# Performance work log

Measured on AMD Instinct MI355X. Metric: run time of the kernel, lower is better.

Reference implementation:

```python
import jax, jax.numpy as jnp
import numpy as np

NOTE_UNITS = 3
NUM_NOTES = 48
NUM_FEATURES = 256
NUM_UNITS = 256
BATCH = 4096


def _uniform(key, shape, k):
    return jax.random.uniform(key, shape, jnp.float32, -k, k)


def setup_inputs() -> dict:
    key = jax.random.key(0)
    ks = jax.random.split(key, 12)
    k = 1.0 / np.sqrt(NUM_UNITS)
    in0 = NUM_FEATURES + NOTE_UNITS  # layer-0 input: features concat shifted notes
    return {
        "note_features": jax.random.normal(ks[0], (BATCH, NUM_NOTES, NUM_FEATURES), jnp.float32),
        "condition_notes": jax.random.uniform(ks[1], (BATCH, NUM_NOTES, NOTE_UNITS), jnp.float32),
        "W_ih0": _uniform(ks[2], (4 * NUM_UNITS, in0), k),
        "W_hh0": _uniform(ks[3], (4 * NUM_UNITS, NUM_UNITS), k),
        "b_ih0": _uniform(ks[4], (4 * NUM_UNITS,), k),
        "b_hh0": _uniform(ks[5], (4 * NUM_UNITS,), k),
        "W_ih1": _uniform(ks[6], (4 * NUM_UNITS, NUM_UNITS), k),
        "W_hh1": _uniform(ks[7], (4 * NUM_UNITS, NUM_UNITS), k),
        "b_ih1": _uniform(ks[8], (4 * NUM_UNITS,), k),
        "b_hh1": _uniform(ks[9], (4 * NUM_UNITS,), k),
        "W_out": _uniform(ks[10], (NOTE_UNITS, NUM_UNITS), k),
        "b_out": _uniform(ks[11], (NOTE_UNITS,), k),
    }


def _lstm_cell(x, h, c, W_ih, W_hh, b_ih, b_hh):
    # torch.nn.LSTMCell gate order: i, f, g, o (each NUM_UNITS rows)
    gates = x @ W_ih.T + h @ W_hh.T + (b_ih + b_hh)
    i, f, g, o = jnp.split(gates, 4, axis=-1)
    c_new = jax.nn.sigmoid(f) * c + jax.nn.sigmoid(i) * jnp.tanh(g)
    h_new = jax.nn.sigmoid(o) * jnp.tanh(c_new)
    return h_new, c_new


def reference(note_features, condition_notes, W_ih0, W_hh0, b_ih0, b_hh0,
              W_ih1, W_hh1, b_ih1, b_hh1, W_out, b_out):
    temperature = 1.0
    B = note_features.shape[0]
    # shift condition notes right by one (teacher forcing)
    zero_pad = jnp.zeros((B, 1, NOTE_UNITS), note_features.dtype)
    shifted = jnp.concatenate([zero_pad, condition_notes], axis=1)[:, :-1]
    x_all = jnp.concatenate([note_features, shifted], axis=2)  # [B, N, F+3]
    xs = jnp.transpose(x_all, (1, 0, 2))  # [N, B, F+3] for scan over notes

    h0 = jnp.zeros((B, NUM_UNITS), note_features.dtype)
    init = (h0, h0, h0, h0)  # (h_l0, c_l0, h_l1, c_l1)

    def step(carry, x_n):
        h0_, c0_, h1_, c1_ = carry
        h0n, c0n = _lstm_cell(x_n, h0_, c0_, W_ih0, W_hh0, b_ih0, b_hh0)
        h1n, c1n = _lstm_cell(h0n, h1_, c1_, W_ih1, W_hh1, b_ih1, b_hh1)
        return (h0n, c0n, h1n, c1n), h1n

    _, hs = jax.lax.scan(step, init, xs)  # [N, B, U]
    hs = jnp.transpose(hs, (1, 0, 2))  # [B, N, U]
    out = hs @ W_out.T + b_out  # [B, N, 3]
    prob = jax.nn.sigmoid(out[:, :, 0:2] / temperature)
    return jnp.concatenate([prob, out[:, :, 2:3]], axis=2)
```

## Files before the change

kernel.cpp:

```cpp
#include <hip/hip_runtime.h>

typedef _Float16 half8 __attribute__((ext_vector_type(8)));
typedef _Float16 half4 __attribute__((ext_vector_type(4)));
typedef float f32x4 __attribute__((ext_vector_type(4)));

#define NSTEP 48
#define MT 16
#define LDX 264
#define LDH0 296
#define LDH1 264

__device__ __forceinline__ float sigm(float x) { return 1.0f / (1.0f + __expf(-x)); }
__device__ __forceinline__ float tanh_f(float x) {
  float ax = fabsf(x);
  float e = __expf(-2.0f * ax);
  float t = (1.0f - e) / (1.0f + e);
  return copysignf(t, x);
}

__global__ void prep_weights(const float* __restrict__ Wih0, const float* __restrict__ Whh0,
                             const float* __restrict__ bih0, const float* __restrict__ bhh0,
                             const float* __restrict__ Wih1, const float* __restrict__ Whh1,
                             const float* __restrict__ bih1, const float* __restrict__ bhh1,
                             _Float16* __restrict__ W0p, _Float16* __restrict__ W1p,
                             float* __restrict__ b0, float* __restrict__ b1) {
  int n = blockIdx.x;
  int c = n >> 8, u = n & 255, w = u >> 4, r = u & 15;
  for (int k = threadIdx.x; k < 544; k += 256) {
    int kt = k >> 5, kk = k & 31, q = kk >> 3, j = kk & 7;
    float val;
    if (k < 256) val = Wih0[n * 259 + k];
    else if (k < 512) val = Whh0[n * 256 + (k - 256)];
    else if (k < 515) val = Wih0[n * 259 + 256 + (k - 512)];
    else val = 0.0f;
    W0p[((((w * 17 + kt) * 4 + c) * 64) + q * 16 + r) * 8 + j] = (_Float16)val;
  }
  for (int k = threadIdx.x; k < 512; k += 256) {
    int kt = k >> 5, kk = k & 31, q = kk >> 3, j = kk & 7;
    float val = (k < 256) ? Wih1[n * 256 + k] : Whh1[n * 256 + (k - 256)];
    W1p[((((w * 16 + kt) * 4 + c) * 64) + q * 16 + r) * 8 + j] = (_Float16)val;
  }
  if (threadIdx.x == 0) { b0[n] = bih0[n] + bhh0[n]; b1[n] = bih1[n] + bhh1[n]; }
}

__global__ __launch_bounds__(1024, 4)
void noteaxis_main(const float* __restrict__ nf, const float* __restrict__ cond,
                   const _Float16* __restrict__ W0p, const _Float16* __restrict__ W1p,
                   const float* __restrict__ b0g, const float* __restrict__ b1g,
                   const float* __restrict__ Wout, const float* __restrict__ bout,
                   float* __restrict__ out) {
  __shared__ __align__(16) _Float16 lds_x[MT][LDX];
  __shared__ __align__(16) _Float16 lds_h0[MT][LDH0];
  __shared__ __align__(16) _Float16 lds_h1[MT][LDH1];
  __shared__ float lds_part[16][MT][3];

  const int tid = threadIdx.x;
  const int w = tid >> 6;
  const int lane = tid & 63;
  const int r = lane & 15;
  const int q = lane >> 4;
  const int u = w * 16 + r;
  const int row0 = blockIdx.x * MT;

  for (int i = tid; i < MT * LDH0; i += 1024) ((_Float16*)lds_h0)[i] = (_Float16)0.0f;
  for (int i = tid; i < MT * LDH1; i += 1024) ((_Float16*)lds_h1)[i] = (_Float16)0.0f;

  float b0c[4], b1c[4];
#pragma unroll
  for (int c = 0; c < 4; ++c) { b0c[c] = b0g[c * 256 + u]; b1c[c] = b1g[c * 256 + u]; }
  const float wov0 = Wout[u], wov1 = Wout[256 + u], wov2 = Wout[512 + u];
  const float bo0 = bout[0], bo1 = bout[1], bo2 = bout[2];

  float c0s[4], c1s[4];
#pragma unroll
  for (int g = 0; g < 4; ++g) { c0s[g] = 0.0f; c1s[g] = 0.0f; }

  const _Float16* pW0 = W0p + (size_t)w * (17 * 4 * 512) + lane * 8;
  const _Float16* pW1 = W1p + (size_t)w * (16 * 4 * 512) + lane * 8;

  f32x4 acc[4];
  half8 Ba[4], Bc[4];

  auto loadW = [&](half8* d, const _Float16* base, int ktc4) {
#pragma unroll
    for (int c = 0; c < 4; ++c) d[c] = *(const half8*)(base + (ktc4 + c) * 512);
  };
  auto mfma4 = [&](half8 a, const half8* B) {
#pragma unroll
    for (int c = 0; c < 4; ++c)
      acc[c] = __builtin_amdgcn_mfma_f32_16x16x32_f16(a, B[c], acc[c], 0, 0, 0);
  };

  __syncthreads();

#pragma unroll 1
  for (int n = 0; n < NSTEP; ++n) {
    {
      const float4 xv = *(const float4*)(nf + ((size_t)(row0 + w) * NSTEP + n) * 256 + lane * 4);
      half4 hx = { (_Float16)xv.x, (_Float16)xv.y, (_Float16)xv.z, (_Float16)xv.w };
      *(half4*)&lds_x[w][lane * 4] = hx;
    }
    if (tid < MT) {
      float s0 = 0.f, s1 = 0.f, s2 = 0.f;
      if (n > 0) {
        const float* cp = cond + ((size_t)(row0 + tid) * NSTEP + (n - 1)) * 3;
        s0 = cp[0]; s1 = cp[1]; s2 = cp[2];
      }
      lds_h0[tid][256] = (_Float16)s0;
      lds_h0[tid][257] = (_Float16)s1;
      lds_h0[tid][258] = (_Float16)s2;
    }
    __syncthreads();

#pragma unroll
    for (int c = 0; c < 4; ++c) { f32x4 bz = {b0c[c], b0c[c], b0c[c], b0c[c]}; acc[c] = bz; }

#pragma unroll 2
    for (int kt = 0; kt < 8; kt += 2) {
      loadW(Ba, pW0, kt * 4);
      loadW(Bc, pW0, kt * 4 + 4);
      mfma4(*(const half8*)&lds_x[r][kt * 32 + q * 8], Ba);
      mfma4(*(const half8*)&lds_x[r][kt * 32 + 32 + q * 8], Bc);
    }
#pragma unroll 2
    for (int kt = 0; kt < 8; kt += 2) {
      loadW(Ba, pW0, 32 + kt * 4);
      loadW(Bc, pW0, 32 + kt * 4 + 4);
      mfma4(*(const half8*)&lds_h0[r][kt * 32 + q * 8], Ba);
      mfma4(*(const half8*)&lds_h0[r][kt * 32 + 32 + q * 8], Bc);
    }
    loadW(Ba, pW0, 64);
    mfma4(*(const half8*)&lds_h0[r][256 + q * 8], Ba);

    __syncthreads();

#pragma unroll
    for (int g = 0; g < 4; ++g) {
      float i_ = acc[0][g], f_ = acc[1][g], g_ = acc[2][g], o_ = acc[3][g];
      float cc = sigm(f_) * c0s[g] + sigm(i_) * tanh_f(g_);
      c0s[g] = cc;
      lds_h0[q * 4 + g][u] = (_Float16)(sigm(o_) * tanh_f(cc));
    }
    __syncthreads();

#pragma unroll
    for (int c = 0; c < 4; ++c) { f32x4 bz = {b1c[c], b1c[c], b1c[c], b1c[c]}; acc[c] = bz; }

#pragma unroll 2
    for (int kt = 0; kt < 8; kt += 2) {
      loadW(Ba, pW1, kt * 4);
      loadW(Bc, pW1, kt * 4 + 4);
      mfma4(*(const half8*)&lds_h0[r][kt * 32 + q * 8], Ba);
      mfma4(*(const half8*)&lds_h0[r][kt * 32 + 32 + q * 8], Bc);
    }
#pragma unroll 2
    for (int kt = 0; kt < 8; kt += 2) {
      loadW(Ba, pW1, 32 + kt * 4);
      loadW(Bc, pW1, 32 + kt * 4 + 4);
      mfma4(*(const half8*)&lds_h1[r][kt * 32 + q * 8], Ba);
      mfma4(*(const half8*)&lds_h1[r][kt * 32 + 32 + q * 8], Bc);
    }

    __syncthreads();

    float part[4][3];
#pragma unroll
    for (int g = 0; g < 4; ++g) {
      float i_ = acc[0][g], f_ = acc[1][g], g_ = acc[2][g], o_ = acc[3][g];
      float cc = sigm(f_) * c1s[g] + sigm(i_) * tanh_f(g_);
      c1s[g] = cc;
      float hh = sigm(o_) * tanh_f(cc);
      lds_h1[q * 4 + g][u] = (_Float16)hh;
      part[g][0] = hh * wov0;
      part[g][1] = hh * wov1;
      part[g][2] = hh * wov2;
    }
#pragma unroll
    for (int g = 0; g < 4; ++g)
#pragma unroll
      for (int ch = 0; ch < 3; ++ch) {
        float p = part[g][ch];
        p += __shfl_xor(p, 1);
        p += __shfl_xor(p, 2);
        p += __shfl_xor(p, 4);
        p += __shfl_xor(p, 8);
        part[g][ch] = p;
      }
    if (r == 0) {
#pragma unroll
      for (int g = 0; g < 4; ++g) {
        int m = q * 4 + g;
        lds_part[w][m][0] = part[g][0];
        lds_part[w][m][1] = part[g][1];
        lds_part[w][m][2] = part[g][2];
      }
    }
    __syncthreads();

    if (tid < MT * 3) {
      int m = tid / 3, ch = tid - m * 3;
      float s = (ch == 0 ? bo0 : (ch == 1 ? bo1 : bo2));
#pragma unroll
      for (int ww = 0; ww < 16; ++ww) s += lds_part[ww][m][ch];
      if (ch < 2) s = 1.0f / (1.0f + __expf(-s));
      out[((size_t)(row0 + m) * NSTEP + n) * 3 + ch] = s;
    }
  }
}

extern "C" void kernel_launch(void* const* d_in, const int* in_sizes, int n_in,
                              void* d_out, int out_size, void* d_ws, size_t ws_size,
                              hipStream_t stream) {
  const float* nf   = (const float*)d_in[0];
  const float* cond = (const float*)d_in[1];
  const float* Wih0 = (const float*)d_in[2];
  const float* Whh0 = (const float*)d_in[3];
  const float* bih0 = (const float*)d_in[4];
  const float* bhh0 = (const float*)d_in[5];
  const float* Wih1 = (const float*)d_in[6];
  const float* Whh1 = (const float*)d_in[7];
  const float* bih1 = (const float*)d_in[8];
  const float* bhh1 = (const float*)d_in[9];
  const float* Wout = (const float*)d_in[10];
  const float* bout = (const float*)d_in[11];
  float* out = (float*)d_out;

  _Float16* W0p = (_Float16*)d_ws;
  _Float16* W1p = W0p + 16 * 17 * 4 * 512;
  float* b0 = (float*)(W1p + 16 * 16 * 4 * 512);
  float* b1 = b0 + 1024;

  prep_weights<<<1024, 256, 0, stream>>>(Wih0, Whh0, bih0, bhh0, Wih1, Whh1, bih1, bhh1, W0p, W1p, b0, b1);
  noteaxis_main<<<256, 1024, 0, stream>>>(nf, cond, W0p, W1p, b0, b1, Wout, bout, out);
}
```

Baseline: 1.363 ms.

## Software-pipeline weight loads with triple buffering and cut per-step barriers

Replaces the paired weight-fragment loads with a three-deep rotating register buffer that prefetches weight tiles three k-steps ahead, including across the layer-0/layer-1 boundary and into the next time step. It prefetches the next note's features from global memory during the current step and moves the x/condition LDS writes and the output reduction into an existing barrier window, cutting per-step barriers from five to three. It also raises wave priority around the MFMA loops and uses a custom barrier macro. The goal is to hide global weight-load latency and barrier stalls, at the cost of more live registers, which could hurt occupancy under the 1024x4 launch bounds.

```diff
diff --git a/kernel.cpp b/kernel.cpp
--- a/kernel.cpp
+++ b/kernel.cpp
@@ -9,6 +9,10 @@
 #define LDX 264
 #define LDH0 296
 #define LDH1 264
+
+#define BAR() do { asm volatile("s_waitcnt lgkmcnt(0)" ::: "memory"); \
+                   __builtin_amdgcn_s_barrier();                      \
+                   __builtin_amdgcn_sched_barrier(0); } while (0)
 
 __device__ __forceinline__ float sigm(float x) { return 1.0f / (1.0f + __expf(-x)); }
 __device__ __forceinline__ float tanh_f(float x) {
@@ -79,60 +83,55 @@
   const _Float16* pW1 = W1p + (size_t)w * (16 * 4 * 512) + lane * 8;
 
   f32x4 acc[4];
-  half8 Ba[4], Bc[4];
-
-  auto loadW = [&](half8* d, const _Float16* base, int ktc4) {
-#pragma unroll
-    for (int c = 0; c < 4; ++c) d[c] = *(const half8*)(base + (ktc4 + c) * 512);
+  half8 Qb[3][4];
+
+  auto loadQ = [&](int buf, const _Float16* base, int t) {
+#pragma unroll
+    for (int c = 0; c < 4; ++c) Qb[buf][c] = *(const half8*)(base + (t * 4 + c) * 512);
   };
-  auto mfma4 = [&](half8 a, const half8* B) {
+  auto mfma4 = [&](half8 a, int buf) {
 #pragma unroll
     for (int c = 0; c < 4; ++c)
-      acc[c] = __builtin_amdgcn_mfma_f32_16x16x32_f16(a, B[c], acc[c], 0, 0, 0);
+      acc[c] = __builtin_amdgcn_mfma_f32_16x16x32_f16(a, Qb[buf][c], acc[c], 0, 0, 0);
   };
 
+  {
+    const float4 xv = *(const float4*)(nf + ((size_t)(row0 + w) * NSTEP + 0) * 256 + lane * 4);
+    half4 hx = { (_Float16)xv.x, (_Float16)xv.y, (_Float16)xv.z, (_Float16)xv.w };
+    *(half4*)&lds_x[w][lane * 4] = hx;
+  }
   __syncthreads();
+
+  loadQ(0, pW0, 0); loadQ(1, pW0, 1); loadQ(2, pW0, 2);
 
 #pragma unroll 1
   for (int n = 0; n < NSTEP; ++n) {
-    {
-      const float4 xv = *(const float4*)(nf + ((size_t)(row0 + w) * NSTEP + n) * 256 + lane * 4);
-      half4 hx = { (_Float16)xv.x, (_Float16)xv.y, (_Float16)xv.z, (_Float16)xv.w };
-      *(half4*)&lds_x[w][lane * 4] = hx;
-    }
+    const int np = (n + 1 < NSTEP) ? n + 1 : n;
+    const float4 xv = *(const float4*)(nf + ((size_t)(row0 + w) * NSTEP + np) * 256 + lane * 4);
+    float s0 = 0.f, s1 = 0.f, s2 = 0.f;
     if (tid < MT) {
-      float s0 = 0.f, s1 = 0.f, s2 = 0.f;
-      if (n > 0) {
-        const float* cp = cond + ((size_t)(row0 + tid) * NSTEP + (n - 1)) * 3;
-        s0 = cp[0]; s1 = cp[1]; s2 = cp[2];
-      }
-      lds_h0[tid][256] = (_Float16)s0;
-      lds_h0[tid][257] = (_Float16)s1;
-      lds_h0[tid][258] = (_Float16)s2;
-    }
-    __syncthreads();
+      const float* cp = cond + ((size_t)(row0 + tid) * NSTEP + n) * 3;
+      s0 = cp[0]; s1 = cp[1]; s2 = cp[2];
+    }
 
 #pragma unroll
     for (int c = 0; c < 4; ++c) { f32x4 bz = {b0c[c], b0c[c], b0c[c], b0c[c]}; acc[c] = bz; }
 
-#pragma unroll 2
-    for (int kt = 0; kt < 8; kt += 2) {
-      loadW(Ba, pW0, kt * 4);
-      loadW(Bc, pW0, kt * 4 + 4);
-      mfma4(*(const half8*)&lds_x[r][kt * 32 + q * 8], Ba);
-      mfma4(*(const half8*)&lds_x[r][kt * 32 + 32 + q * 8], Bc);
-    }
-#pragma unroll 2
-    for (int kt = 0; kt < 8; kt += 2) {
-      loadW(Ba, pW0, 32 + kt * 4);
-      loadW(Bc, pW0, 32 + kt * 4 + 4);
-      mfma4(*(const half8*)&lds_h0[r][kt * 32 + q * 8], Ba);
-      mfma4(*(const half8*)&lds_h0[r][kt * 32 + 32 + q * 8], Bc);
-    }
-    loadW(Ba, pW0, 64);
-    mfma4(*(const half8*)&lds_h0[r][256 + q * 8], Ba);
-
-    __syncthreads();
+    __builtin_amdgcn_s_setprio(1);
+#pragma unroll
+    for (int t = 0; t < 17; ++t) {
+      half8 a;
+      if (t < 8)       a = *(const half8*)&lds_x[r][t * 32 + q * 8];
+      else if (t < 16) a = *(const half8*)&lds_h0[r][(t - 8) * 32 + q * 8];
+      else             a = *(const half8*)&lds_h0[r][256 + q * 8];
+      mfma4(a, t % 3);
+      const int nt = t + 3;
+      if (nt < 17) loadQ(t % 3, pW0, nt);
+      else         loadQ(t % 3, pW1, nt - 17);
+    }
+    __builtin_amdgcn_s_setprio(0);
+
+    BAR();
 
 #pragma unroll
     for (int g = 0; g < 4; ++g) {
@@ -141,27 +140,42 @@
       c0s[g] = cc;
       lds_h0[q * 4 + g][u] = (_Float16)(sigm(o_) * tanh_f(cc));
     }
-    __syncthreads();
+    {
+      half4 hx = { (_Float16)xv.x, (_Float16)xv.y, (_Float16)xv.z, (_Float16)xv.w };
+      *(half4*)&lds_x[w][lane * 4] = hx;
+    }
+    if (tid < MT) {
+      lds_h0[tid][256] = (_Float16)s0;
+      lds_h0[tid][257] = (_Float16)s1;
+      lds_h0[tid][258] = (_Float16)s2;
+    }
+    if (n > 0 && tid < MT * 3) {
+      int m = tid / 3, ch = tid - m * 3;
+      float s = (ch == 0 ? bo0 : (ch == 1 ? bo1 : bo2));
+#pragma unroll
+      for (int ww = 0; ww < 16; ++ww) s += lds_part[ww][m][ch];
+      if (ch < 2) s = 1.0f / (1.0f + __expf(-s));
+      out[((size_t)(row0 + m) * NSTEP + (n - 1)) * 3 + ch] = s;
+    }
+
+    BAR();
 
 #pragma unroll
     for (int c = 0; c < 4; ++c) { f32x4 bz = {b1c[c], b1c[c], b1c[c], b1c[c]}; acc[c] = bz; }
 
-#pragma unroll 2
-    for (int kt = 0; kt < 8; kt += 2) {
-      loadW(Ba, pW1, kt * 4);
-      loadW(Bc, pW1, kt * 4 + 4);
-      mfma4(*(const half8*)&lds_h0[r][kt * 32 + q * 8], Ba);
-      mfma4(*(const half8*)&lds_h0[r][kt * 32 + 32 + q * 8], Bc);
-    }
-#pragma unroll 2
-    for (int kt = 0; kt < 8; kt += 2) {
-      loadW(Ba, pW1, 32 + kt * 4);
-      loadW(Bc, pW1, 32 + kt * 4 + 4);
-      mfma4(*(const half8*)&lds_h1[r][kt * 32 + q * 8], Ba);
-      mfma4(*(const half8*)&lds_h1[r][kt * 32 + 32 + q * 8], Bc);
-    }
-
-    __syncthreads();
+    __builtin_amdgcn_s_setprio(1);
+#pragma unroll
+    for (int t = 0; t < 16; ++t) {
+      half8 a = (t < 8) ? *(const half8*)&lds_h0[r][t * 32 + q * 8]
+                        : *(const half8*)&lds_h1[r][(t - 8) * 32 + q * 8];
+      mfma4(a, (t + 2) % 3);
+      const int nt = t + 3;
+      if (nt < 16) loadQ((t + 2) % 3, pW1, nt);
+      else         loadQ((t + 2) % 3, pW0, nt - 16);
+    }
+    __builtin_amdgcn_s_setprio(0);
+
+    BAR();
 
     float part[4][3];
 #pragma unroll
@@ -195,16 +209,16 @@
         lds_part[w][m][2] = part[g][2];
       }
     }
-    __syncthreads();
-
-    if (tid < MT * 3) {
-      int m = tid / 3, ch = tid - m * 3;
-      float s = (ch == 0 ? bo0 : (ch == 1 ? bo1 : bo2));
-#pragma unroll
-      for (int ww = 0; ww < 16; ++ww) s += lds_part[ww][m][ch];
-      if (ch < 2) s = 1.0f / (1.0f + __expf(-s));
-      out[((size_t)(row0 + m) * NSTEP + n) * 3 + ch] = s;
-    }
+  }
+
+  BAR();
+  if (tid < MT * 3) {
+    int m = tid / 3, ch = tid - m * 3;
+    float s = (ch == 0 ? bo0 : (ch == 1 ? bo1 : bo2));
+#pragma unroll
+    for (int ww = 0; ww < 16; ++ww) s += lds_part[ww][m][ch];
+    if (ch < 2) s = 1.0f / (1.0f + __expf(-s));
+    out[((size_t)(row0 + m) * NSTEP + (NSTEP - 1)) * 3 + ch] = s;
   }
 }
 
```

Measured after the change: 5.158 ms. 3.78x slower.

## Process 32 batch rows per block to reuse each weight fragment twice

Applied to the files above, without the earlier changes.

Doubles the rows per workgroup from 16 to 32 so every weight fragment loaded from global memory feeds two MFMA row tiles, with separate accumulators and cell states for each half. The grid is halved to 128 blocks, and the gate biases are staged in LDS instead of registers. This targets the per-step weight-streaming cost, but uses only half the CUs and raises register pressure.

```diff
diff --git a/kernel.cpp b/kernel.cpp
--- a/kernel.cpp
+++ b/kernel.cpp
@@ -5,7 +5,7 @@
 typedef float f32x4 __attribute__((ext_vector_type(4)));
 
 #define NSTEP 48
-#define MT 16
+#define MT 32
 #define LDX 264
 #define LDH0 296
 #define LDH1 264
@@ -53,6 +53,7 @@
   __shared__ __align__(16) _Float16 lds_h0[MT][LDH0];
   __shared__ __align__(16) _Float16 lds_h1[MT][LDH1];
   __shared__ float lds_part[16][MT][3];
+  __shared__ float lds_b0[1024], lds_b1[1024];
 
   const int tid = threadIdx.x;
   const int w = tid >> 6;
@@ -64,31 +65,32 @@
 
   for (int i = tid; i < MT * LDH0; i += 1024) ((_Float16*)lds_h0)[i] = (_Float16)0.0f;
   for (int i = tid; i < MT * LDH1; i += 1024) ((_Float16*)lds_h1)[i] = (_Float16)0.0f;
-
-  float b0c[4], b1c[4];
-#pragma unroll
-  for (int c = 0; c < 4; ++c) { b0c[c] = b0g[c * 256 + u]; b1c[c] = b1g[c * 256 + u]; }
+  lds_b0[tid] = b0g[tid];
+  lds_b1[tid] = b1g[tid];
+
   const float wov0 = Wout[u], wov1 = Wout[256 + u], wov2 = Wout[512 + u];
   const float bo0 = bout[0], bo1 = bout[1], bo2 = bout[2];
 
-  float c0s[4], c1s[4];
-#pragma unroll
-  for (int g = 0; g < 4; ++g) { c0s[g] = 0.0f; c1s[g] = 0.0f; }
+  float c0sA[4], c0sB[4], c1sA[4], c1sB[4];
+#pragma unroll
+  for (int g = 0; g < 4; ++g) { c0sA[g] = 0.0f; c0sB[g] = 0.0f; c1sA[g] = 0.0f; c1sB[g] = 0.0f; }
 
   const _Float16* pW0 = W0p + (size_t)w * (17 * 4 * 512) + lane * 8;
   const _Float16* pW1 = W1p + (size_t)w * (16 * 4 * 512) + lane * 8;
 
-  f32x4 acc[4];
+  f32x4 accA[4], accB[4];
   half8 Ba[4], Bc[4];
 
   auto loadW = [&](half8* d, const _Float16* base, int ktc4) {
 #pragma unroll
     for (int c = 0; c < 4; ++c) d[c] = *(const half8*)(base + (ktc4 + c) * 512);
   };
-  auto mfma4 = [&](half8 a, const half8* B) {
-#pragma unroll
-    for (int c = 0; c < 4; ++c)
-      acc[c] = __builtin_amdgcn_mfma_f32_16x16x32_f16(a, B[c], acc[c], 0, 0, 0);
+  auto mfmaD = [&](half8 aA, half8 aB, const half8* B) {
+#pragma unroll
+    for (int c = 0; c < 4; ++c) {
+      accA[c] = __builtin_amdgcn_mfma_f32_16x16x32_f16(aA, B[c], accA[c], 0, 0, 0);
+      accB[c] = __builtin_amdgcn_mfma_f32_16x16x32_f16(aB, B[c], accB[c], 0, 0, 0);
+    }
   };
 
   __syncthreads();
@@ -96,9 +98,12 @@
 #pragma unroll 1
   for (int n = 0; n < NSTEP; ++n) {
     {
-      const float4 xv = *(const float4*)(nf + ((size_t)(row0 + w) * NSTEP + n) * 256 + lane * 4);
-      half4 hx = { (_Float16)xv.x, (_Float16)xv.y, (_Float16)xv.z, (_Float16)xv.w };
-      *(half4*)&lds_x[w][lane * 4] = hx;
+      const float4 xa = *(const float4*)(nf + ((size_t)(row0 + w) * NSTEP + n) * 256 + lane * 4);
+      const float4 xb = *(const float4*)(nf + ((size_t)(row0 + 16 + w) * NSTEP + n) * 256 + lane * 4);
+      half4 ha = { (_Float16)xa.x, (_Float16)xa.y, (_Float16)xa.z, (_Float16)xa.w };
+      half4 hb = { (_Float16)xb.x, (_Float16)xb.y, (_Float16)xb.z, (_Float16)xb.w };
+      *(half4*)&lds_x[w][lane * 4] = ha;
+      *(half4*)&lds_x[16 + w][lane * 4] = hb;
     }
     if (tid < MT) {
       float s0 = 0.f, s1 = 0.f, s2 = 0.f;
@@ -113,95 +118,123 @@
     __syncthreads();
 
 #pragma unroll
-    for (int c = 0; c < 4; ++c) { f32x4 bz = {b0c[c], b0c[c], b0c[c], b0c[c]}; acc[c] = bz; }
+    for (int c = 0; c < 4; ++c) {
+      float b = lds_b0[c * 256 + u];
+      f32x4 bz = {b, b, b, b};
+      accA[c] = bz; accB[c] = bz;
+    }
 
 #pragma unroll 2
     for (int kt = 0; kt < 8; kt += 2) {
       loadW(Ba, pW0, kt * 4);
       loadW(Bc, pW0, kt * 4 + 4);
-      mfma4(*(const half8*)&lds_x[r][kt * 32 + q * 8], Ba);
-      mfma4(*(const half8*)&lds_x[r][kt * 32 + 32 + q * 8], Bc);
+      mfmaD(*(const half8*)&lds_x[r][kt * 32 + q * 8],
+            *(const half8*)&lds_x[16 + r][kt * 32 + q * 8], Ba);
+      mfmaD(*(const half8*)&lds_x[r][kt * 32 + 32 + q * 8],
+            *(const half8*)&lds_x[16 + r][kt * 32 + 32 + q * 8], Bc);
     }
 #pragma unroll 2
     for (int kt = 0; kt < 8; kt += 2) {
       loadW(Ba, pW0, 32 + kt * 4);
       loadW(Bc, pW0, 32 + kt * 4 + 4);
-      mfma4(*(const half8*)&lds_h0[r][kt * 32 + q * 8], Ba);
-      mfma4(*(const half8*)&lds_h0[r][kt * 32 + 32 + q * 8], Bc);
+      mfmaD(*(const half8*)&lds_h0[r][kt * 32 + q * 8],
+            *(const half8*)&lds_h0[16 + r][kt * 32 + q * 8], Ba);
+      mfmaD(*(const half8*)&lds_h0[r][kt * 32 + 32 + q * 8],
+            *(const half8*)&lds_h0[16 + r][kt * 32 + 32 + q * 8], Bc);
     }
     loadW(Ba, pW0, 64);
-    mfma4(*(const half8*)&lds_h0[r][256 + q * 8], Ba);
+    mfmaD(*(const half8*)&lds_h0[r][256 + q * 8],
+          *(const half8*)&lds_h0[16 + r][256 + q * 8], Ba);
 
     __syncthreads();
 
 #pragma unroll
     for (int g = 0; g < 4; ++g) {
-      float i_ = acc[0][g], f_ = acc[1][g], g_ = acc[2][g], o_ = acc[3][g];
-      float cc = sigm(f_) * c0s[g] + sigm(i_) * tanh_f(g_);
-      c0s[g] = cc;
-      lds_h0[q * 4 + g][u] = (_Float16)(sigm(o_) * tanh_f(cc));
-    }
-    __syncthreads();
-
-#pragma unroll
-    for (int c = 0; c < 4; ++c) { f32x4 bz = {b1c[c], b1c[c], b1c[c], b1c[c]}; acc[c] = bz; }
+      float iA = accA[0][g], fA = accA[1][g], gA = accA[2][g], oA = accA[3][g];
+      float ccA = sigm(fA) * c0sA[g] + sigm(iA) * tanh_f(gA);
+      c0sA[g] = ccA;
+      lds_h0[q * 4 + g][u] = (_Float16)(sigm(oA) * tanh_f(ccA));
+      float iB = accB[0][g], fB = accB[1][g], gB = accB[2][g], oB = accB[3][g];
+      float ccB = sigm(fB) * c0sB[g] + sigm(iB) * tanh_f(gB);
+      c0sB[g] = ccB;
+      lds_h0[16 + q * 4 + g][u] = (_Float16)(sigm(oB) * tanh_f(ccB));
+    }
+    __syncthreads();
+
+#pragma unroll
+    for (int c = 0; c < 4; ++c) {
+      float b = lds_b1[c * 256 + u];
+      f32x4 bz = {b, b, b, b};
+      accA[c] = bz; accB[c] = bz;
+    }
 
 #pragma unroll 2
     for (int kt = 0; kt < 8; kt += 2) {
       loadW(Ba, pW1, kt * 4);
       loadW(Bc, pW1, kt * 4 + 4);
-      mfma4(*(const half8*)&lds_h0[r][kt * 32 + q * 8], Ba);
-      mfma4(*(const half8*)&lds_h0[r][kt * 32 + 32 + q * 8], Bc);
+      mfmaD(*(const half8*)&lds_h0[r][kt * 32 + q * 8],
+            *(const half8*)&lds_h0[16 + r][kt * 32 + q * 8], Ba);
+      mfmaD(*(const half8*)&lds_h0[r][kt * 32 + 32 + q * 8],
+            *(const half8*)&lds_h0[16 + r][kt * 32 + 32 + q * 8], Bc);
     }
 #pragma unroll 2
     for (int kt = 0; kt < 8; kt += 2) {
       loadW(Ba, pW1, 32 + kt * 4);
       loadW(Bc, pW1, 32 + kt * 4 + 4);
-      mfma4(*(const half8*)&lds_h1[r][kt * 32 + q * 8], Ba);
-      mfma4(*(const half8*)&lds_h1[r][kt * 32 + 32 + q * 8], Bc);
-    }
-
-    __syncthreads();
-
-    float part[4][3];
-#pragma unroll
-    for (int g = 0; g < 4; ++g) {
-      float i_ = acc[0][g], f_ = acc[1][g], g_ = acc[2][g], o_ = acc[3][g];
-      float cc = sigm(f_) * c1s[g] + sigm(i_) * tanh_f(g_);
-      c1s[g] = cc;
-      float hh = sigm(o_) * tanh_f(cc);
-      lds_h1[q * 4 + g][u] = (_Float16)hh;
-      part[g][0] = hh * wov0;
-      part[g][1] = hh * wov1;
-      part[g][2] = hh * wov2;
-    }
-#pragma unroll
-    for (int g = 0; g < 4; ++g)
-#pragma unroll
-      for (int ch = 0; ch < 3; ++ch) {
-        float p = part[g][ch];
-        p += __shfl_xor(p, 1);
-        p += __shfl_xor(p, 2);
-        p += __shfl_xor(p, 4);
-        p += __shfl_xor(p, 8);
-        part[g][ch] = p;
+      mfmaD(*(const half8*)&lds_h1[r][kt * 32 + q * 8],
+            *(const half8*)&lds_h1[16 + r][kt * 32 + q * 8], Ba);
+      mfmaD(*(const half8*)&lds_h1[r][kt * 32 + 32 + q * 8],
+            *(const half8*)&lds_h1[16 + r][kt * 32 + 32 + q * 8], Bc);
+    }
+
+    __syncthreads();
+
+#pragma unroll
+    for (int grp = 0; grp < 2; ++grp) {
+      float part[4][3];
+#pragma unroll
+      for (int g = 0; g < 4; ++g) {
+        float i_, f_, g_, o_, cprev;
+        if (grp == 0) { i_ = accA[0][g]; f_ = accA[1][g]; g_ = accA[2][g]; o_ = accA[3][g]; cprev = c1sA[g]; }
+        else          { i_ = accB[0][g]; f_ = accB[1][g]; g_ = accB[2][g]; o_ = accB[3][g]; cprev = c1sB[g]; }
+        float cc = sigm(f_) * cprev + sigm(i_) * tanh_f(g_);
+        if (grp == 0) c1sA[g] = cc; else c1sB[g] = cc;
+        float hh = sigm(o_) * tanh_f(cc);
+        lds_h1[grp * 16 + q * 4 + g][u] = (_Float16)hh;
+        part[g][0] = hh * wov0;
+        part[g][1] = hh * wov1;
+        part[g][2] = hh * wov2;
       }
-    if (r == 0) {
-#pragma unroll
-      for (int g = 0; g < 4; ++g) {
-        int m = q * 4 + g;
-        lds_part[w][m][0] = part[g][0];
-        lds_part[w][m][1] = part[g][1];
-        lds_part[w][m][2] = part[g][2];
+#pragma unroll
+      for (int g = 0; g < 4; ++g)
+#pragma unroll
+        for (int ch = 0; ch < 3; ++ch) {
+          float p = part[g][ch];
+          p += __shfl_xor(p, 1);
+          p += __shfl_xor(p, 2);
+          p += __shfl_xor(p, 4);
+          p += __shfl_xor(p, 8);
+          part[g][ch] = p;
+        }
+      if (r == 0) {
+#pragma unroll
+        for (int g = 0; g < 4; ++g) {
+          int m = grp * 16 + q * 4 + g;
+          lds_part[w][m][0] = part[g][0];
+          lds_part[w][m][1] = part[g][1];
+          lds_part[w][m][2] = part[g][2];
+        }
       }
     }
     __syncthreads();
 
     if (tid < MT * 3) {
-      int m = tid / 3, ch = tid - m * 3;
-      float s = (ch == 0 ? bo0 : (ch == 1 ? bo1 : bo2));
-#pragma unroll
-      for (int ww = 0; ww < 16; ++ww) s += lds_part[ww][m][ch];
+      int m = tid / 3;
+      int ch = tid - m * 3;
+      float s = lds_part[0][m][ch];
+#pragma unroll
+      for (int ww = 1; ww < 16; ++ww) s += lds_part[ww][m][ch];
+      s += (ch == 0 ? bo0 : (ch == 1 ? bo1 : bo2));
       if (ch < 2) s = 1.0f / (1.0f + __expf(-s));
       out[((size_t)(row0 + m) * NSTEP + n) * 3 + ch] = s;
     }
@@ -231,5 +264,5 @@
   float* b1 = b0 + 1024;
 
   prep_weights<<<1024, 256, 0, stream>>>(Wih0, Whh0, bih0, bhh0, Wih1, Whh1, bih1, bhh1, W0p, W1p, b0, b1);
-  noteaxis_main<<<256, 1024, 0, stream>>>(nf, cond, W0p, W1p, b0, b1, Wout, bout, out);
-}
+  noteaxis_main<<<128, 1024, 0, stream>>>(nf, cond, W0p, W1p, b0, b1, Wout, bout, out);
+}
```

Result: slower. 1.730 ms (+26.9%).
